# Optimization experiments

Hardware: AMD Instinct MI355X
Metric: run time of the kernel (lower is better)

Reference implementation:

```python
import jax, jax.numpy as jnp
import numpy as np

DIM = 4096
N_HEADS = 32
N_KV_HEADS = 8
HEAD_DIM = DIM // N_HEADS  # 128
N_REP = N_HEADS // N_KV_HEADS  # 4
THETA = 10000.0
B, S = 4, 1024


def setup_inputs() -> dict:
    key = jax.random.key(0)
    ks = jax.random.split(key, 5)
    sc = 1.0 / np.sqrt(DIM).astype(np.float32)
    x = jax.random.normal(ks[0], (B, S, DIM), jnp.float32)
    wq = jax.random.normal(ks[1], (DIM, N_HEADS * HEAD_DIM), jnp.float32) * sc
    wk = jax.random.normal(ks[2], (DIM, N_KV_HEADS * HEAD_DIM), jnp.float32) * sc
    wv = jax.random.normal(ks[3], (DIM, N_KV_HEADS * HEAD_DIM), jnp.float32) * sc
    wo = jax.random.normal(ks[4], (N_HEADS * HEAD_DIM, DIM), jnp.float32) * sc
    return {"x": x, "wq": wq, "wk": wk, "wv": wv, "wo": wo}


def _rope_cos_sin(seq_len):
    # matches precompute_freqs_cis: freqs over even indices, angles = t * freqs
    freqs = 1.0 / (THETA ** (jnp.arange(0, HEAD_DIM, 2, dtype=jnp.float32) / HEAD_DIM))
    t = jnp.arange(seq_len, dtype=jnp.float32)
    ang = jnp.outer(t, freqs)  # [S, HEAD_DIM//2]
    return jnp.cos(ang), jnp.sin(ang)


def _apply_rope(x, cos, sin):
    # x: [B, S, H, D]; consecutive pairs form complex numbers (view_as_complex)
    xr = x[..., 0::2]
    xi = x[..., 1::2]
    c = cos[None, :, None, :]
    s = sin[None, :, None, :]
    out_r = xr * c - xi * s
    out_i = xr * s + xi * c
    return jnp.stack([out_r, out_i], axis=-1).reshape(x.shape)


def reference(x, wq, wk, wv, wo):
    bsz, seq_len, _ = x.shape
    q = (x @ wq).reshape(bsz, seq_len, N_HEADS, HEAD_DIM)
    k = (x @ wk).reshape(bsz, seq_len, N_KV_HEADS, HEAD_DIM)
    v = (x @ wv).reshape(bsz, seq_len, N_KV_HEADS, HEAD_DIM)
    cos, sin = _rope_cos_sin(seq_len)
    q = _apply_rope(q, cos, sin)
    k = _apply_rope(k, cos, sin)
    # repeat_kv: expand each kv head N_REP times contiguously
    k = jnp.repeat(k, N_REP, axis=2)
    v = jnp.repeat(v, N_REP, axis=2)
    scores = jnp.einsum('bqhd,bkhd->bhqk', q, k) / np.float32(np.sqrt(HEAD_DIM))
    mask = jnp.triu(jnp.full((seq_len, seq_len), -jnp.inf, dtype=scores.dtype), k=1)
    scores = scores + mask
    attn = jax.nn.softmax(scores.astype(jnp.float32), axis=-1).astype(q.dtype)
    out = jnp.einsum('bhqk,bkhd->bqhd', attn, v).reshape(bsz, seq_len, N_HEADS * HEAD_DIM)
    return out @ wo
```

## Files before the change

### kernel.cpp

```cpp
#include <hip/hip_runtime.h>

typedef unsigned short u16;
typedef unsigned int u32;
typedef __attribute__((ext_vector_type(8))) short short8_t;
typedef __attribute__((ext_vector_type(4))) float f32x4;

static constexpr int Bc = 4, Sc = 1024, Hc = 32, HKVc = 8, Dc = 128;
static constexpr int BS = Bc * Sc;
static constexpr int DIMc = 4096;

__device__ __forceinline__ u16 f2bf(float f) {
  u32 u = __float_as_uint(f);
  u32 r = (u + 0x7fffu + ((u >> 16) & 1u)) >> 16;
  return (u16)r;
}
__device__ __forceinline__ float bf2f(u16 u) {
  return __uint_as_float(((u32)u) << 16);
}
__device__ __forceinline__ void gload_lds16(const void* g, void* l) {
  __builtin_amdgcn_global_load_lds((const __attribute__((address_space(1))) void*)g,
                                   (__attribute__((address_space(3))) void*)l, 16, 0, 0);
}

#define SBAR __builtin_amdgcn_sched_barrier(0)
#define PBARRIER do { SBAR; __builtin_amdgcn_s_barrier(); SBAR; } while (0)
#define WAITVM(N) asm volatile("s_waitcnt vmcnt(" #N ")" ::: "memory")

__global__ void rope_table_k(float* __restrict__ tbl) {
  int i = blockIdx.x * 256 + threadIdx.x;
  int s = i >> 6, fi = i & 63;
  float freq = powf(10000.f, -(float)fi / 64.f);
  float ang = (float)s * freq;
  float sv, cv;
  sincosf(ang, &sv, &cv);
  tbl[2 * i] = cv;
  tbl[2 * i + 1] = sv;
}

__global__ void f32_to_bf16_k(const float* __restrict__ in, u16* __restrict__ out, int n4) {
  int i = blockIdx.x * 256 + threadIdx.x;
  if (i >= n4) return;
  float4 v = *(const float4*)(in + (size_t)i * 4);
  uint2 pk;
  pk.x = (u32)f2bf(v.x) | ((u32)f2bf(v.y) << 16);
  pk.y = (u32)f2bf(v.z) | ((u32)f2bf(v.w) << 16);
  *(uint2*)(out + (size_t)i * 4) = pk;
}

__global__ __launch_bounds__(256) void transpose_w_k(const float* __restrict__ W, u16* __restrict__ WT,
                                                     int Kdim, int Ndim) {
  __shared__ float tile[64 * 65];
  const int t = threadIdx.x;
  const int n0 = blockIdx.x * 64, k0 = blockIdx.y * 64;
  #pragma unroll
  for (int p = 0; p < 4; ++p) {
    int idx = p * 256 + t;
    int r = idx >> 4, c = (idx & 15) * 4;
    float4 v = *(const float4*)(W + (size_t)(k0 + r) * Ndim + n0 + c);
    tile[r * 65 + c + 0] = v.x;
    tile[r * 65 + c + 1] = v.y;
    tile[r * 65 + c + 2] = v.z;
    tile[r * 65 + c + 3] = v.w;
  }
  __syncthreads();
  #pragma unroll
  for (int p = 0; p < 2; ++p) {
    int idx = p * 256 + t;
    int n = idx >> 3, c = (idx & 7) * 8;
    alignas(16) u16 o[8];
    #pragma unroll
    for (int i = 0; i < 8; ++i) o[i] = f2bf(tile[(c + i) * 65 + n]);
    *(uint4*)(WT + (size_t)(n0 + n) * Kdim + k0 + c) = *(const uint4*)o;
  }
}

#define MFMAQ(QI)                                                                        \
  do {                                                                                   \
    __builtin_amdgcn_s_setprio(1);                                                       \
    _Pragma("unroll") for (int mf = 0; mf < 4; ++mf)                                     \
      _Pragma("unroll") for (int nf = 0; nf < 2; ++nf)                                   \
        _Pragma("unroll") for (int kk = 0; kk < 2; ++kk)                                 \
          acc[QI][mf][nf] = __builtin_amdgcn_mfma_f32_16x16x32_bf16(                     \
              af[mf][kk], bf[nf][kk], acc[QI][mf][nf], 0, 0, 0);                         \
    __builtin_amdgcn_s_setprio(0);                                                       \
  } while (0)

template <int MODE>
__global__ __launch_bounds__(512, 2) void gemm256(const u16* __restrict__ A, const u16* __restrict__ BT,
                                                  void* __restrict__ Cv, const float* __restrict__ tbl,
                                                  int M, int N, int K) {
  extern __shared__ char smem[];
  const int t = threadIdx.x, l = t & 63, w = t >> 6;
  const int ln15 = l & 15, lh = l >> 4;
  const int NT = K >> 6;

  int id = blockIdx.x;
  int nwg = gridDim.x;
  int swz = ((nwg & 7) == 0) ? ((id & 7) * (nwg >> 3) + (id >> 3)) : id;
  const int nbn = N >> 8;
  const int bm = swz / nbn, bn = swz % nbn;

  const u16* Ag = A + (size_t)bm * 256 * K;
  const u16* Bg = BT + (size_t)bn * 256 * K;

  f32x4 acc[4][4][2];
  #pragma unroll
  for (int q = 0; q < 4; ++q)
    #pragma unroll
    for (int mf = 0; mf < 4; ++mf)
      #pragma unroll
      for (int nf = 0; nf < 2; ++nf) acc[q][mf][nf] = f32x4{0.f, 0.f, 0.f, 0.f};
  short8_t af[4][2], bf[2][2];

  const int srow = (l >> 3);
  const int sck  = (l & 7) ^ srow;
  auto stageA = [&](char* bufbase, int h, int tt) {
    char* lb = bufbase + h * 16384 + w * 1024;
    const u16* g = Ag + (size_t)(h * 128 + w * 8 + srow) * K + tt * 64 + (sck << 3);
    gload_lds16(g, lb);
    gload_lds16(g + (size_t)64 * K, lb + 8192);
  };
  auto stageB = [&](char* bufbase, int h, int tt) {
    char* lb = bufbase + 32768 + h * 16384 + w * 1024;
    const u16* g = Bg + (size_t)(h * 128 + w * 8 + srow) * K + tt * 64 + (sck << 3);
    gload_lds16(g, lb);
    gload_lds16(g + (size_t)64 * K, lb + 8192);
  };
  const int arow = (w >> 2) * 64 + ln15;
  const int brow = (w & 3) * 32 + ln15;
  const int rsw = ln15 & 7;
  auto LDA = [&](const char* cb, int qm) {
    #pragma unroll
    for (int mf = 0; mf < 4; ++mf)
      #pragma unroll
      for (int kk = 0; kk < 2; ++kk)
        af[mf][kk] = *(const short8_t*)(cb + qm * 16384 + (arow + mf * 16) * 128 +
                                        (((kk * 4 + lh) ^ rsw) << 4));
  };
  auto LDB = [&](const char* cb, int qn) {
    #pragma unroll
    for (int nf = 0; nf < 2; ++nf)
      #pragma unroll
      for (int kk = 0; kk < 2; ++kk)
        bf[nf][kk] = *(const short8_t*)(cb + 32768 + qn * 16384 + (brow + nf * 16) * 128 +
                                        (((kk * 4 + lh) ^ rsw) << 4));
  };

  {
    char* b0 = smem;
    char* b1 = smem + 65536;
    stageB(b0, 0, 0);
    stageA(b0, 1, 0);
    stageA(b0, 0, 0);
    stageB(b0, 1, 0);
    stageB(b1, 0, 1);
    stageA(b1, 1, 1);
  }
  WAITVM(6);
  PBARRIER;

  for (int T = 0; T < NT - 1; ++T) {
    char* cb = smem + (T & 1) * 65536;
    char* nb = smem + ((T & 1) ^ 1) * 65536;
    LDA(cb, 0); LDB(cb, 0);
    stageA(nb, 0, T + 1);
    PBARRIER;
    MFMAQ(0);
    PBARRIER;
    LDA(cb, 1);
    stageB(nb, 1, T + 1);
    PBARRIER;
    MFMAQ(1);
    WAITVM(8);
    PBARRIER;
    LDB(cb, 1);
    if (T + 2 < NT) stageB(cb, 0, T + 2);
    PBARRIER;
    MFMAQ(2);
    PBARRIER;
    LDA(cb, 0);
    if (T + 2 < NT) stageA(cb, 1, T + 2);
    PBARRIER;
    MFMAQ(3);
    if (T + 2 < NT) { WAITVM(6); }
    else            { WAITVM(2); }
    PBARRIER;
  }
  {
    char* cb = smem + ((NT - 1) & 1) * 65536;
    LDA(cb, 0); LDB(cb, 0);
    PBARRIER; MFMAQ(0); PBARRIER;
    LDA(cb, 1);
    PBARRIER; MFMAQ(1);
    WAITVM(0);
    PBARRIER;
    LDB(cb, 1);
    PBARRIER; MFMAQ(2); PBARRIER;
    LDA(cb, 0);
    PBARRIER; MFMAQ(3);
  }

  const int rw = (w >> 2) * 64, cw = (w & 3) * 32;
  #pragma unroll
  for (int qi = 0; qi < 4; ++qi) {
    const int qm = (qi == 1 || qi == 2) ? 1 : 0;
    const int qn = (qi >= 2) ? 1 : 0;
    #pragma unroll
    for (int mf = 0; mf < 4; ++mf)
      #pragma unroll
      for (int nf = 0; nf < 2; ++nf)
        #pragma unroll
        for (int e = 0; e < 4; ++e) {
          int row = bm * 256 + qm * 128 + rw + mf * 16 + lh * 4 + e;
          int col = bn * 256 + qn * 128 + cw + nf * 16 + ln15;
          float v = acc[qi][mf][nf][e];
          if (MODE == 2) {
            float pv = __shfl_xor(v, 1);
            int d = col & 127, hh = col >> 7;
            int s = row & (Sc - 1), bb = row >> 10;
            float2 cs = *(const float2*)(tbl + (size_t)(s * 64 + (d >> 1)) * 2);
            float o = (d & 1) ? (v * cs.x + pv * cs.y) : (v * cs.x - pv * cs.y);
            o *= 0.08838834764831845f;
            ((u16*)Cv)[(((size_t)(bb * Hc + hh) * Sc + s) << 7) + d] = f2bf(o);
          } else {
            size_t idx = (size_t)row * N + col;
            ((float*)Cv)[idx] = v;
          }
        }
  }
}

#define MFMAKV(QM)                                                                       \
  do {                                                                                   \
    __builtin_amdgcn_s_setprio(1);                                                       \
    _Pragma("unroll") for (int mf = 0; mf < 4; ++mf)                                     \
      _Pragma("unroll") for (int nf = 0; nf < 2; ++nf)                                   \
        _Pragma("unroll") for (int kk = 0; kk < 2; ++kk)                                 \
          acc[QM][mf][nf] = __builtin_amdgcn_mfma_f32_16x16x32_bf16(                     \
              af[mf][kk], bf[nf][kk], acc[QM][mf][nf], 0, 0, 0);                         \
    __builtin_amdgcn_s_setprio(0);                                                       \
  } while (0)

__global__ __launch_bounds__(512, 1) void gemm_kv(const u16* __restrict__ A, const u16* __restrict__ BT,
                                                  u16* __restrict__ Krp, u16* __restrict__ Vtp,
                                                  const float* __restrict__ tbl) {
  extern __shared__ char smem[];
  const int t = threadIdx.x, l = t & 63, w = t >> 6;
  const int ln15 = l & 15, lh = l >> 4;
  const int K = 4096, NT = 64;

  int id = blockIdx.x;
  int swz = (id & 7) * 32 + (id >> 3);
  const int bm = swz >> 4, bn = swz & 15;

  const u16* Ag = A + (size_t)bm * 256 * K;
  const u16* Bg = BT + (size_t)bn * 128 * K;

  f32x4 acc[2][4][2];
  #pragma unroll
  for (int q = 0; q < 2; ++q)
    #pragma unroll
    for (int mf = 0; mf < 4; ++mf)
      #pragma unroll
      for (int nf = 0; nf < 2; ++nf) acc[q][mf][nf] = f32x4{0.f, 0.f, 0.f, 0.f};
  short8_t af[4][2], bf[2][2];

  const int srow = (l >> 3);
  const int sck  = (l & 7) ^ srow;
  auto stageA = [&](int buf, int h, int tt) {
    char* lb = smem + buf * 32768 + h * 16384 + w * 2048;
    const u16* g = Ag + (size_t)(h * 128 + w * 16 + srow) * K + tt * 64 + (sck << 3);
    gload_lds16(g, lb);
    gload_lds16(g + (size_t)8 * K, lb + 1024);
  };
  auto stageB = [&](int buf, int tt) {
    char* lb = smem + 65536 + buf * 16384 + w * 2048;
    const u16* g = Bg + (size_t)(w * 16 + srow) * K + tt * 64 + (sck << 3);
    gload_lds16(g, lb);
    gload_lds16(g + (size_t)8 * K, lb + 1024);
  };
  const int arow = (w >> 2) * 64 + ln15;
  const int brow = (w & 3) * 32 + ln15;
  const int rsw = ln15 & 7;
  auto LDA = [&](int buf, int qm) {
    #pragma unroll
    for (int mf = 0; mf < 4; ++mf)
      #pragma unroll
      for (int kk = 0; kk < 2; ++kk)
        af[mf][kk] = *(const short8_t*)(smem + buf * 32768 + qm * 16384 + (arow + mf * 16) * 128 +
                                        (((kk * 4 + lh) ^ rsw) << 4));
  };
  auto LDB = [&](int buf) {
    #pragma unroll
    for (int nf = 0; nf < 2; ++nf)
      #pragma unroll
      for (int kk = 0; kk < 2; ++kk)
        bf[nf][kk] = *(const short8_t*)(smem + 65536 + buf * 16384 + (brow + nf * 16) * 128 +
                                        (((kk * 4 + lh) ^ rsw) << 4));
  };

  stageA(0, 0, 0);
  stageB(0, 0);
  stageA(0, 1, 0);
  WAITVM(2);
  PBARRIER;

  for (int T = 0; T < NT; ++T) {
    const int cb = T & 1, nb = cb ^ 1;
    const bool st = (T + 1 < NT);
    LDA(cb, 0); LDB(cb);
    if (st) stageA(nb, 0, T + 1);
    PBARRIER;
    MFMAKV(0);
    if (st) { WAITVM(2); } else { WAITVM(0); }
    PBARRIER;
    LDA(cb, 1);
    if (st) { stageB(nb, T + 1); stageA(nb, 1, T + 1); }
    PBARRIER;
    MFMAKV(1);
    if (st) { WAITVM(2); }
    PBARRIER;
  }

  #pragma unroll
  for (int qm = 0; qm < 2; ++qm)
    #pragma unroll
    for (int mf = 0; mf < 4; ++mf)
      #pragma unroll
      for (int nf = 0; nf < 2; ++nf)
        #pragma unroll
        for (int e = 0; e < 4; ++e) {
          int row = bm * 256 + qm * 128 + (w >> 2) * 64 + mf * 16 + lh * 4 + e;
          int col = bn * 128 + (w & 3) * 32 + nf * 16 + ln15;
          float v = acc[qm][mf][nf][e];
          float pv = __shfl_xor(v, 1);
          int s = row & (Sc - 1), bb = row >> 10;
          if (col < 1024) {
            int hkv = col >> 7, d = col & 127;
            float2 cs = *(const float2*)(tbl + (size_t)(s * 64 + (d >> 1)) * 2);
            float o = (d & 1) ? (v * cs.x + pv * cs.y) : (v * cs.x - pv * cs.y);
            Krp[(((size_t)(bb * HKVc + hkv) * Sc + s) << 7) + d] = f2bf(o);
          } else {
            int vc = col - 1024;
            int hkv = vc >> 7, d = vc & 127;
            int sl = s & 63;
            int sg = (sl & 32) | (((sl >> 2) & 3) << 3) | (((sl >> 4) & 1) << 2) | (sl & 3);
            Vtp[((size_t)(bb * HKVc + hkv) * Dc + d) * Sc + (s & ~63) + sg] = f2bf(v);
          }
        }
}

__global__ __launch_bounds__(512, 4) void attn_k(const u16* __restrict__ Q, const u16* __restrict__ Kr,
                                                 const u16* __restrict__ Vt, u16* __restrict__ AO) {
  extern __shared__ char smem[];
  const int t = threadIdx.x, l = t & 63, w = t >> 6;
  const int qb = (int)gridDim.x - 1 - (int)blockIdx.x;
  const int h = blockIdx.y, b = blockIdx.z;
  const int hkv = h >> 2;
  const int ln15 = l & 15, lh = l >> 4;
  const int NT = 2 * qb + 2;

  const u16* Kg0 = Kr + (size_t)(b * HKVc + hkv) * Sc * Dc;
  const u16* Vg0 = Vt + (size_t)(b * HKVc + hkv) * Dc * Sc;

  auto stageK = [&](int buf, int tt) {
    char* base = smem + buf * 16384 + w * 2048;
    #pragma unroll
    for (int i = 0; i < 2; ++i) {
      int row = w * 8 + i * 4 + (l >> 4);
      int c = l & 15;
      gload_lds16(Kg0 + (size_t)(tt * 64 + row) * Dc + ((c ^ (row & 7)) << 3), base + i * 1024);
    }
  };
  auto stageV = [&](int buf, int tt) {
    char* base = smem + 32768 + buf * 16384 + w * 2048;
    #pragma unroll
    for (int i = 0; i < 2; ++i) {
      int d = w * 16 + i * 8 + (l >> 3);
      int c = l & 7;
      gload_lds16(Vg0 + (size_t)d * Sc + tt * 64 + ((c ^ (d & 7)) << 3), base + i * 1024);
    }
  };

  short8_t qf[4];
  {
    int q = qb * 128 + w * 16 + ln15;
    const u16* qp = Q + ((size_t)(b * Hc + h) * Sc + q) * Dc + lh * 8;
    #pragma unroll
    for (int ks = 0; ks < 4; ++ks) qf[ks] = *(const short8_t*)(qp + ks * 32);
  }
  SBAR;

  f32x4 oacc[8];
  #pragma unroll
  for (int i = 0; i < 8; ++i) oacc[i] = f32x4{0.f, 0.f, 0.f, 0.f};
  float mrun = -1e30f, lrun = 0.f;

  stageK(0, 0); stageV(0, 0);
  stageK(1, 1); stageV(1, 1);

  const int qmaxw = qb * 128 + w * 16 + 15;
  const int qlane = qb * 128 + w * 16 + ln15;

  for (int T = 0; T < NT; ++T) {
    if (T < NT - 1) { WAITVM(4); } else { WAITVM(0); }
    PBARRIER;
    const char* Kb = smem + (T & 1) * 16384;
    const char* Vb = smem + 32768 + (T & 1) * 16384;

    if (T * 64 <= qmaxw) {
      f32x4 sf[4];
      #pragma unroll
      for (int fc = 0; fc < 4; ++fc) {
        sf[fc] = f32x4{0.f, 0.f, 0.f, 0.f};
        int kvr = fc * 16 + ln15;
        #pragma unroll
        for (int ks = 0; ks < 4; ++ks) {
          int chunk = ks * 4 + lh;
          short8_t kf = *(const short8_t*)(Kb + kvr * 256 + ((chunk ^ (kvr & 7)) << 4));
          sf[fc] = __builtin_amdgcn_mfma_f32_16x16x32_bf16(kf, qf[ks], sf[fc], 0, 0, 0);
        }
      }
      if (T * 64 + 63 > qb * 128 + w * 16) {
        #pragma unroll
        for (int fc = 0; fc < 4; ++fc)
          #pragma unroll
          for (int j = 0; j < 4; ++j) {
            int kvg = T * 64 + fc * 16 + lh * 4 + j;
            if (kvg > qlane) sf[fc][j] = -1e30f;
          }
      }
      float mx = sf[0][0];
      #pragma unroll
      for (int fc = 0; fc < 4; ++fc)
        #pragma unroll
        for (int j = 0; j < 4; ++j) mx = fmaxf(mx, sf[fc][j]);
      mx = fmaxf(mx, __shfl_xor(mx, 16));
      mx = fmaxf(mx, __shfl_xor(mx, 32));
      float mnew = fmaxf(mrun, mx);
      float alpha = __expf(mrun - mnew);
      mrun = mnew;
      float rs = 0.f;
      #pragma unroll
      for (int fc = 0; fc < 4; ++fc)
        #pragma unroll
        for (int j = 0; j < 4; ++j) {
          float p = __expf(sf[fc][j] - mnew);
          sf[fc][j] = p;
          rs += p;
        }
      rs += __shfl_xor(rs, 16);
      rs += __shfl_xor(rs, 32);
      lrun = lrun * alpha + rs;
      float arow[4];
      #pragma unroll
      for (int j = 0; j < 4; ++j) arow[j] = __shfl(alpha, (l & 48) | (lh * 4 + j));
      #pragma unroll
      for (int fd = 0; fd < 8; ++fd)
        #pragma unroll
        for (int j = 0; j < 4; ++j) oacc[fd][j] *= arow[j];
      short8_t pa[2];
      #pragma unroll
      for (int ks = 0; ks < 2; ++ks)
        #pragma unroll
        for (int b2 = 0; b2 < 2; ++b2)
          #pragma unroll
          for (int j = 0; j < 4; ++j) pa[ks][b2 * 4 + j] = (short)f2bf(sf[ks * 2 + b2][j]);
      #pragma unroll
      for (int fd = 0; fd < 8; ++fd) {
        int dcol = fd * 16 + ln15;
        #pragma unroll
        for (int ks = 0; ks < 2; ++ks) {
          int chunk = ks * 4 + lh;
          short8_t vf = *(const short8_t*)(Vb + dcol * 128 + ((chunk ^ (dcol & 7)) << 4));
          oacc[fd] = __builtin_amdgcn_mfma_f32_16x16x32_bf16(pa[ks], vf, oacc[fd], 0, 0, 0);
        }
      }
    }
    PBARRIER;
    if (T + 2 < NT) { stageK(T & 1, T + 2); stageV(T & 1, T + 2); }
  }

  float linv[4];
  #pragma unroll
  for (int j = 0; j < 4; ++j) linv[j] = 1.f / __shfl(lrun, (l & 48) | (lh * 4 + j));
  #pragma unroll
  for (int j = 0; j < 4; ++j) {
    int q = qb * 128 + w * 16 + lh * 4 + j;
    u16* op = AO + (size_t)(b * Sc + q) * DIMc + h * Dc + ln15;
    #pragma unroll
    for (int fd = 0; fd < 8; ++fd) op[fd * 16] = f2bf(oacc[fd][j] * linv[j]);
  }
}

extern "C" void kernel_launch(void* const* d_in, const int* in_sizes, int n_in,
                              void* d_out, int out_size, void* d_ws, size_t ws_size,
                              hipStream_t stream) {
  const float* x  = (const float*)d_in[0];
  const float* wq = (const float*)d_in[1];
  const float* wk = (const float*)d_in[2];
  const float* wv = (const float*)d_in[3];
  const float* wo = (const float*)d_in[4];
  float* out = (float*)d_out;

  char* ws = (char*)d_ws;
  size_t off = 0;
  auto alloc = [&](size_t bytes) -> char* {
    char* p = ws + off;
    off += (bytes + 255) & ~(size_t)255;
    return p;
  };
  float* tbl  = (float*)alloc((size_t)Sc * 64 * 2 * 4);
  u16* xb    = (u16*)alloc((size_t)BS * DIMc * 2);
  u16* wqT   = (u16*)alloc((size_t)4096 * 4096 * 2);
  u16* wkvT  = (u16*)alloc((size_t)2048 * 4096 * 2);
  u16* Qb    = (u16*)alloc((size_t)BS * 4096 * 2);
  u16* Krp   = (u16*)alloc((size_t)BS * 1024 * 2);
  u16* Vtp   = (u16*)alloc((size_t)BS * 1024 * 2);
  u16* AO = xb;
  u16* woT = wqT;

  rope_table_k<<<(Sc * 64) / 256, 256, 0, stream>>>(tbl);
  f32_to_bf16_k<<<(BS * DIMc / 4) / 256, 256, 0, stream>>>(x, xb, BS * DIMc / 4);

  transpose_w_k<<<dim3(64, 64), 256, 0, stream>>>(wq, wqT, 4096, 4096);
  gemm256<2><<<256, 512, 131072, stream>>>(xb, wqT, Qb, tbl, 4096, 4096, 4096);

  transpose_w_k<<<dim3(16, 64), 256, 0, stream>>>(wk, wkvT, 4096, 1024);
  transpose_w_k<<<dim3(16, 64), 256, 0, stream>>>(wv, wkvT + (size_t)1024 * 4096, 4096, 1024);
  gemm_kv<<<256, 512, 98304, stream>>>(xb, wkvT, Krp, Vtp, tbl);

  attn_k<<<dim3(8, Hc, Bc), 512, 65536, stream>>>(Qb, Krp, Vtp, AO);

  transpose_w_k<<<dim3(64, 64), 256, 0, stream>>>(wo, woT, 4096, 4096);
  gemm256<1><<<256, 512, 131072, stream>>>(AO, woT, out, tbl, 4096, 4096, 4096);
}
```

Baseline: 494.9 us.

## Restage GEMM prefetch schedule and drop barriers between LDS reads and MFMA

Reworks the double-buffered GEMM main loop so the next B half-tile is staged earlier, the peeled last iteration is merged into the loop with guard flags, and several workgroup barriers between LDS fragment loads and MFMA blocks are removed. The KV-projection loop likewise drops the barriers that separated staging from MFMA. The aim is fewer stalls and more overlap of global-to-LDS loads with matrix math. In exchange, the altered wait counts and fewer barriers raise the risk of read/write races on the LDS buffers.

```diff
diff --git a/kernel.cpp b/kernel.cpp
--- a/kernel.cpp
+++ b/kernel.cpp
@@ -155,49 +155,33 @@
     stageB(b0, 1, 0);
     stageB(b1, 0, 1);
     stageA(b1, 1, 1);
+    stageB(b1, 1, 1);
   }
   WAITVM(6);
   PBARRIER;
 
-  for (int T = 0; T < NT - 1; ++T) {
+  for (int T = 0; T < NT; ++T) {
     char* cb = smem + (T & 1) * 65536;
     char* nb = smem + ((T & 1) ^ 1) * 65536;
+    const bool s1 = (T + 1 < NT), s2 = (T + 2 < NT);
     LDA(cb, 0); LDB(cb, 0);
-    stageA(nb, 0, T + 1);
-    PBARRIER;
+    if (s1) stageA(nb, 0, T + 1);
     MFMAQ(0);
     PBARRIER;
     LDA(cb, 1);
-    stageB(nb, 1, T + 1);
-    PBARRIER;
+    if (s2) stageB(cb, 0, T + 2);
     MFMAQ(1);
-    WAITVM(8);
     PBARRIER;
     LDB(cb, 1);
-    if (T + 2 < NT) stageB(cb, 0, T + 2);
-    PBARRIER;
+    if (s2) stageA(cb, 1, T + 2);
     MFMAQ(2);
     PBARRIER;
     LDA(cb, 0);
-    if (T + 2 < NT) stageA(cb, 1, T + 2);
-    PBARRIER;
+    if (s2) stageB(cb, 1, T + 2);
     MFMAQ(3);
-    if (T + 2 < NT) { WAITVM(6); }
-    else            { WAITVM(2); }
-    PBARRIER;
-  }
-  {
-    char* cb = smem + ((NT - 1) & 1) * 65536;
-    LDA(cb, 0); LDB(cb, 0);
-    PBARRIER; MFMAQ(0); PBARRIER;
-    LDA(cb, 1);
-    PBARRIER; MFMAQ(1);
-    WAITVM(0);
-    PBARRIER;
-    LDB(cb, 1);
-    PBARRIER; MFMAQ(2); PBARRIER;
-    LDA(cb, 0);
-    PBARRIER; MFMAQ(3);
+    if (s2)      { WAITVM(6); }
+    else if (s1) { WAITVM(0); }
+    PBARRIER;
   }
 
   const int rw = (w >> 2) * 64, cw = (w & 3) * 32;
@@ -310,13 +294,11 @@
     const bool st = (T + 1 < NT);
     LDA(cb, 0); LDB(cb);
     if (st) stageA(nb, 0, T + 1);
-    PBARRIER;
     MFMAKV(0);
     if (st) { WAITVM(2); } else { WAITVM(0); }
     PBARRIER;
     LDA(cb, 1);
     if (st) { stageB(nb, T + 1); stageA(nb, 1, T + 1); }
-    PBARRIER;
     MFMAKV(1);
     if (st) { WAITVM(2); }
     PBARRIER;
```

Result: no change. 487.1 us (-1.6%).
